# Optimization experiments

Hardware: AMD Instinct MI355X
Metric: run time of the kernel (lower is better)

## Reference

```python
import jax, jax.numpy as jnp
import numpy as np

WH, WW = 8, 8
NUM_HEADS = 8
DIM = 256
MLP_HIDDEN = 1024
EPS = 1e-5


def _rel_pos_index(wh, ww):
    ch, cw = np.meshgrid(np.arange(wh), np.arange(ww), indexing='ij')
    flat = np.stack([ch.ravel(), cw.ravel()])            # (2, N)
    rel = flat[:, :, None] - flat[:, None, :]            # (2, N, N)
    rel = rel.transpose(1, 2, 0).copy()                  # (N, N, 2)
    rel[:, :, 0] += wh - 1
    rel[:, :, 1] += ww - 1
    rel[:, :, 0] *= 2 * ww - 1
    return jnp.asarray(rel.sum(-1))                      # (N, N) int

REL_IDX = _rel_pos_index(WH, WW)


def _layernorm(x, g, b):
    mu = x.mean(-1, keepdims=True)
    var = ((x - mu) ** 2).mean(-1, keepdims=True)
    return (x - mu) * jax.lax.rsqrt(var + EPS) * g + b


def _window_partition(x):
    B, H, W, C = x.shape
    x = x.reshape(B, H // WH, WH, W // WW, WW, C)
    return x.transpose(0, 1, 3, 2, 4, 5).reshape(-1, WH * WW, C)


def _window_reverse(w, B, H, W):
    C = w.shape[-1]
    x = w.reshape(B, H // WH, W // WW, WH, WW, C)
    return x.transpose(0, 1, 3, 2, 4, 5).reshape(B, H, W, C)


def _window_attn(qx, kvx, qw, qb, kvw, kvb, bias_table, pw, pb):
    # qx/kvx: [Bw, N, C]; weights stored as [in, out] (torch Linear transposed)
    Bw, N, C = qx.shape
    hd = C // NUM_HEADS
    scale = hd ** -0.5
    q = (qx @ qw + qb).reshape(Bw, N, NUM_HEADS, hd).transpose(0, 2, 1, 3) * scale
    kv = (kvx @ kvw + kvb).reshape(Bw, N, 2, NUM_HEADS, hd)
    k = kv[:, :, 0].transpose(0, 2, 1, 3)
    v = kv[:, :, 1].transpose(0, 2, 1, 3)
    attn = jnp.einsum('bhnd,bhmd->bhnm', q, k)
    bias = bias_table[REL_IDX.reshape(-1)].reshape(N, N, NUM_HEADS).transpose(2, 0, 1)
    attn = jax.nn.softmax(attn + bias[None], axis=-1)
    out = jnp.einsum('bhnm,bhmd->bhnd', attn, v).transpose(0, 2, 1, 3).reshape(Bw, N, C)
    return out @ pw + pb


def setup_inputs() -> dict:
    key = jax.random.key(0)
    ks = jax.random.split(key, 16)
    B, H, W, C = 4, 160, 160, DIM
    nW = (H // WH) * (W // WW)
    N = WH * WW
    n_bias = (2 * WH - 1) * (2 * WW - 1)  # 225
    s = 0.02
    return {
        'x': jax.random.normal(ks[0], (B, H, W, C), jnp.float32),
        'enc_feat': jax.random.normal(ks[1], (B, H, W, C), jnp.float32),
        'mask_matrix': jnp.zeros((nW, N, N), jnp.float32),
        'norm1_g': jnp.ones((C,), jnp.float32),
        'norm1_b': jnp.zeros((C,), jnp.float32),
        'q1_w': jax.random.normal(ks[2], (C, C), jnp.float32) * s,
        'q1_b': jnp.zeros((C,), jnp.float32),
        'kv1_w': jax.random.normal(ks[3], (C, 2 * C), jnp.float32) * s,
        'kv1_b': jnp.zeros((2 * C,), jnp.float32),
        'bias1': jax.random.normal(ks[4], (n_bias, NUM_HEADS), jnp.float32) * s,
        'proj1_w': jax.random.normal(ks[5], (C, C), jnp.float32) * s,
        'proj1_b': jnp.zeros((C,), jnp.float32),
        'q2_w': jax.random.normal(ks[6], (C, C), jnp.float32) * s,
        'q2_b': jnp.zeros((C,), jnp.float32),
        'kv2_w': jax.random.normal(ks[7], (C, 2 * C), jnp.float32) * s,
        'kv2_b': jnp.zeros((2 * C,), jnp.float32),
        'bias2': jax.random.normal(ks[8], (n_bias, NUM_HEADS), jnp.float32) * s,
        'proj2_w': jax.random.normal(ks[9], (C, C), jnp.float32) * s,
        'proj2_b': jnp.zeros((C,), jnp.float32),
        'norm2_g': jnp.ones((C,), jnp.float32),
        'norm2_b': jnp.zeros((C,), jnp.float32),
        'fc1_w': jax.random.normal(ks[10], (C, MLP_HIDDEN), jnp.float32) * s,
        'fc1_b': jnp.zeros((MLP_HIDDEN,), jnp.float32),
        'fc2_w': jax.random.normal(ks[11], (MLP_HIDDEN, C), jnp.float32) * s,
        'fc2_b': jnp.zeros((C,), jnp.float32),
    }


def reference(x, enc_feat, mask_matrix, norm1_g, norm1_b, q1_w, q1_b, kv1_w, kv1_b,
              bias1, proj1_w, proj1_b, q2_w, q2_b, kv2_w, kv2_b, bias2, proj2_w,
              proj2_b, norm2_g, norm2_b, fc1_w, fc1_b, fc2_w, fc2_b):
    # NOTE: the source forward never passes mask_matrix into attention; faithful here.
    B, H, W, C = x.shape
    shortcut = x
    xn = _layernorm(x, norm1_g, norm1_b)
    xw = _window_partition(xn)              # [B*nW, N, C]
    ew = _window_partition(enc_feat)        # [B*nW, N, C]
    # windowed self-attention with relative position bias
    xw = _window_attn(xw, xw, q1_w, q1_b, kv1_w, kv1_b, bias1, proj1_w, proj1_b)
    # windowed cross-attention to encoder features
    xw = _window_attn(xw, ew, q2_w, q2_b, kv2_w, kv2_b, bias2, proj2_w, proj2_b)
    x = shortcut + _window_reverse(xw, B, H, W)
    h = _layernorm(x, norm2_g, norm2_b)
    h = jax.nn.gelu(h @ fc1_w + fc1_b, approximate=False) @ fc2_w + fc2_b
    return x + h
```

## Files before the change

kernel.cpp:

```cpp
#include <hip/hip_runtime.h>

typedef __attribute__((ext_vector_type(4))) float f32x4;
typedef __attribute__((ext_vector_type(8))) short bf16x8;
typedef __attribute__((ext_vector_type(8))) unsigned short ushort8;
typedef unsigned short u16;
typedef unsigned int u32;

#define LDS_AS(p) ((__attribute__((address_space(3))) void*)(p))
#define GLB_AS(p) ((const __attribute__((address_space(1))) void*)(p))

__device__ __forceinline__ u16 f2b(float f) {
    u32 u = __builtin_bit_cast(u32, f);
    u32 r = (u + 0x7fffu + ((u >> 16) & 1u)) >> 16;
    return (u16)r;
}
__device__ __forceinline__ float b2f(u16 u) {
    return __builtin_bit_cast(float, (u32)u << 16);
}

struct PrepAll {
    const float* src[8];
    u16* dst[8];
    int K[8];
    int N[8];
    float S[8];
};

__global__ __launch_bounds__(256) void prep_w(PrepAll p) {
    const int wi = blockIdx.y;
    const int K = p.K[wi], N = p.N[wi];
    for (int e = blockIdx.x * 256 + threadIdx.x; e < K * N; e += gridDim.x * 256) {
        const int k = e / N, n = e % N;
        p.dst[wi][n * K + k] = f2b(p.src[wi][e] * p.S[wi]);
    }
}

__global__ __launch_bounds__(256) void prep_bias(const float* __restrict__ t1,
                                                 const float* __restrict__ t2,
                                                 float* __restrict__ Bm) {
    const int hh = blockIdx.x;
    const int s = hh >> 3, h = hh & 7;
    const float* tab = s ? t2 : t1;
    const int j = threadIdx.x & 63;
    for (int i = threadIdx.x >> 6; i < 64; i += 4) {
        const int idx = ((i >> 3) - (j >> 3) + 7) * 15 + ((i & 7) - (j & 7) + 7);
        Bm[(long)hh * 4096 + i * 64 + j] = tab[idx * 8 + h];
    }
}

__global__ __launch_bounds__(256) void prep_bcat(const float* __restrict__ q1b,
                                                 const float* __restrict__ q2b,
                                                 float qs, float* __restrict__ q1bs,
                                                 float* __restrict__ q2bs) {
    const int g = threadIdx.x;
    q1bs[g] = qs * q1b[g];
    q2bs[g] = qs * q2b[g];
}

__global__ __launch_bounds__(256) void cast_bf(const float* __restrict__ in,
                                               u16* __restrict__ out, long n8) {
    for (long i = (long)blockIdx.x * 256 + threadIdx.x; i < n8; i += (long)gridDim.x * 256) {
        const float4 a = *(const float4*)(in + i * 8);
        const float4 b = *(const float4*)(in + i * 8 + 4);
        ushort8 o;
        o[0] = f2b(a.x); o[1] = f2b(a.y); o[2] = f2b(a.z); o[3] = f2b(a.w);
        o[4] = f2b(b.x); o[5] = f2b(b.y); o[6] = f2b(b.z); o[7] = f2b(b.w);
        *(ushort8*)(out + i * 8) = o;
    }
}

__global__ __launch_bounds__(256) void ln256(const float* __restrict__ x,
                                             const float* __restrict__ g,
                                             const float* __restrict__ b,
                                             u16* __restrict__ out) {
    const int lane = threadIdx.x & 63;
    const int c = lane * 4;
    const float4 gv = *(const float4*)(g + c);
    const float4 bv = *(const float4*)(b + c);
#pragma unroll
    for (int it = 0; it < 8; ++it) {
        const long row = (long)blockIdx.x * 32 + it * 4 + (threadIdx.x >> 6);
        const float4 v = *(const float4*)(x + row * 256 + c);
        float s = v.x + v.y + v.z + v.w;
        float s2 = v.x * v.x + v.y * v.y + v.z * v.z + v.w * v.w;
#pragma unroll
        for (int off = 32; off > 0; off >>= 1) {
            s += __shfl_xor(s, off);
            s2 += __shfl_xor(s2, off);
        }
        const float mu = s * (1.f / 256.f);
        const float rr = rsqrtf(s2 * (1.f / 256.f) - mu * mu + 1e-5f);
        ushort4 o;
        o.x = f2b((v.x - mu) * rr * gv.x + bv.x);
        o.y = f2b((v.y - mu) * rr * gv.y + bv.y);
        o.z = f2b((v.z - mu) * rr * gv.z + bv.z);
        o.w = f2b((v.w - mu) * rr * gv.w + bv.w);
        *(ushort4*)(out + row * 256 + c) = o;
    }
}

__global__ __launch_bounds__(256) void ln_add(const float* __restrict__ x,
                                              const u16* __restrict__ p,
                                              const float* __restrict__ g,
                                              const float* __restrict__ b,
                                              float* __restrict__ out,
                                              u16* __restrict__ xo) {
    const int lane = threadIdx.x & 63;
    const int c = lane * 4;
    const float4 gv = *(const float4*)(g + c);
    const float4 bv = *(const float4*)(b + c);
#pragma unroll
    for (int it = 0; it < 8; ++it) {
        const long row = (long)blockIdx.x * 32 + it * 4 + (threadIdx.x >> 6);
        float4 v = *(const float4*)(x + row * 256 + c);
        const ushort4 pb = *(const ushort4*)(p + row * 256 + c);
        v.x += b2f(pb.x); v.y += b2f(pb.y); v.z += b2f(pb.z); v.w += b2f(pb.w);
        *(float4*)(out + row * 256 + c) = v;
        float s = v.x + v.y + v.z + v.w;
        float s2 = v.x * v.x + v.y * v.y + v.z * v.z + v.w * v.w;
#pragma unroll
        for (int off = 32; off > 0; off >>= 1) {
            s += __shfl_xor(s, off);
            s2 += __shfl_xor(s2, off);
        }
        const float mu = s * (1.f / 256.f);
        const float rr = rsqrtf(s2 * (1.f / 256.f) - mu * mu + 1e-5f);
        ushort4 o;
        o.x = f2b((v.x - mu) * rr * gv.x + bv.x);
        o.y = f2b((v.y - mu) * rr * gv.y + bv.y);
        o.z = f2b((v.z - mu) * rr * gv.z + bv.z);
        o.w = f2b((v.w - mu) * rr * gv.w + bv.w);
        *(ushort4*)(xo + row * 256 + c) = o;
    }
}

template <int SAME>
__global__ __launch_bounds__(512, 2) void attn_f(const u16* __restrict__ xq,
                                                 const u16* __restrict__ xkv,
                                                 const u16* __restrict__ wq,
                                                 const u16* __restrict__ wkv,
                                                 const float* __restrict__ bq,
                                                 const float* __restrict__ bkv,
                                                 const u16* __restrict__ wp,
                                                 const float* __restrict__ bp,
                                                 const float* __restrict__ Bm,
                                                 u16* __restrict__ OUT) {
    __shared__ u16 LDS[38912];
    const int t = threadIdx.x, lane = t & 63, h = t >> 6;
    const int l15 = lane & 15, lg = lane >> 4;

    const int w = blockIdx.x;
    const int b = w / 400, rem = w % 400;
    const int wy = rem / 20, wx = rem % 20;
    const long base_t = (long)b * 25600 + wy * 1280 + wx * 8;
    auto trow = [&](int r) -> long { return base_t + (r >> 3) * 160 + (r & 7); };

#pragma unroll
    for (int j = 0; j < 4; j++) {
        const int row = j * 16 + (t >> 5);
        const int c0 = t & 31, sc = c0 ^ (row & 7);
        __builtin_amdgcn_global_load_lds(GLB_AS(xq + trow(row) * 256 + sc * 8),
                                         LDS_AS(&LDS[(j * 512 + t) * 8]), 16, 0, 0);
    }
    if (!SAME) {
#pragma unroll
        for (int j = 0; j < 4; j++) {
            const int row = j * 16 + (t >> 5);
            const int c0 = t & 31, sc = c0 ^ (row & 7);
            __builtin_amdgcn_global_load_lds(GLB_AS(xkv + trow(row) * 256 + sc * 8),
                                             LDS_AS(&LDS[16384 + (j * 512 + t) * 8]), 16, 0, 0);
        }
    }
    asm volatile("s_waitcnt vmcnt(0)" ::: "memory");
    __builtin_amdgcn_s_barrier();

    constexpr int XKV = SAME ? 0 : 16384;
    const f32x4 zz = (f32x4){0.f, 0.f, 0.f, 0.f};

    f32x4 aQ[4][2], aK[4][2], aV[4][2];
#pragma unroll
    for (int mi = 0; mi < 4; mi++)
#pragma unroll
        for (int n = 0; n < 2; n++) { aQ[mi][n] = zz; aK[mi][n] = zz; aV[mi][n] = zz; }

    const u16* wv = wkv + 256 * 256;

#define QKV_PASS(ACC, W, XB)                                                               \
    do {                                                                                   \
        _Pragma("unroll") for (int s = 0; s < 8; s++) {                                    \
            bf16x8 wf0 = *(const bf16x8*)((W) + (h * 32 + l15) * 256 + s * 32 + lg * 8);   \
            bf16x8 wf1 = *(const bf16x8*)((W) + (h * 32 + 16 + l15) * 256 + s * 32 + lg * 8); \
            bf16x8 af[4];                                                                  \
            _Pragma("unroll") for (int mi = 0; mi < 4; mi++)                               \
                af[mi] = *(const bf16x8*)&LDS[(XB) + ((mi * 16 + l15) * 32 +               \
                                              ((s * 4 + lg) ^ (l15 & 7))) * 8];            \
            _Pragma("unroll") for (int mi = 0; mi < 4; mi++) {                             \
                ACC[mi][0] = __builtin_amdgcn_mfma_f32_16x16x32_bf16(af[mi], wf0, ACC[mi][0], 0, 0, 0); \
                ACC[mi][1] = __builtin_amdgcn_mfma_f32_16x16x32_bf16(af[mi], wf1, ACC[mi][1], 0, 0, 0); \
            }                                                                              \
        }                                                                                  \
    } while (0)

    QKV_PASS(aQ, wq, 0);
    QKV_PASS(aK, wkv, XKV);
    QKV_PASS(aV, wv, XKV);
#undef QKV_PASS
    __builtin_amdgcn_s_barrier();

    float bQ[2], bK[2], bV[2];
#pragma unroll
    for (int n = 0; n < 2; n++) {
        bQ[n] = bq[h * 32 + n * 16 + l15];
        bK[n] = bkv[h * 32 + n * 16 + l15];
        bV[n] = bkv[256 + h * 32 + n * 16 + l15];
    }

    const int SB = h * 4864;
#pragma unroll
    for (int mi = 0; mi < 4; mi++)
#pragma unroll
        for (int n = 0; n < 2; n++)
#pragma unroll
            for (int r = 0; r < 4; r++)
                LDS[SB + 2560 + (n * 16 + l15) * 72 + mi * 16 + lg * 4 + r] = f2b(aV[mi][n][r] + bV[n]);

#pragma unroll
    for (int mi = 0; mi < 4; mi++)
#pragma unroll
        for (int n = 0; n < 2; n++)
#pragma unroll
            for (int r = 0; r < 4; r++)
                LDS[SB + (mi * 16 + lg * 4 + r) * 40 + n * 16 + l15] = f2b(aQ[mi][n][r] + bQ[n]);
    bf16x8 qf[4];
#pragma unroll
    for (int ti = 0; ti < 4; ti++)
        qf[ti] = *(const bf16x8*)&LDS[SB + (ti * 16 + l15) * 40 + lg * 8];
#pragma unroll
    for (int mi = 0; mi < 4; mi++)
#pragma unroll
        for (int n = 0; n < 2; n++)
#pragma unroll
            for (int r = 0; r < 4; r++)
                LDS[SB + (mi * 16 + lg * 4 + r) * 40 + n * 16 + l15] = f2b(aK[mi][n][r] + bK[n]);
    bf16x8 kf[4];
#pragma unroll
    for (int ti = 0; ti < 4; ti++)
        kf[ti] = *(const bf16x8*)&LDS[SB + (ti * 16 + l15) * 40 + lg * 8];

    f32x4 s4[4][4];
#pragma unroll
    for (int ti = 0; ti < 4; ti++)
#pragma unroll
        for (int tj = 0; tj < 4; tj++)
            s4[ti][tj] = __builtin_amdgcn_mfma_f32_16x16x32_bf16(qf[ti], kf[tj], zz, 0, 0, 0);

    const float* Bh = Bm + h * 4096;
    f32x4 o[4][2];
#pragma unroll
    for (int mi = 0; mi < 4; mi++)
#pragma unroll
        for (int n = 0; n < 2; n++) o[mi][n] = zz;

#pragma unroll
    for (int hf = 0; hf < 2; ++hf) {
#pragma unroll
        for (int ti = 0; ti < 4; ti++) {
#pragma unroll
            for (int r = 0; r < 4; r++) {
                const int i = ti * 16 + lg * 4 + r;
                float vv[4];
                float m = -1e30f;
#pragma unroll
                for (int tj = 0; tj < 4; tj++) {
                    vv[tj] = s4[ti][tj][r] + Bh[i * 64 + tj * 16 + l15];
                    m = fmaxf(m, vv[tj]);
                }
#pragma unroll
                for (int off = 1; off < 16; off <<= 1) m = fmaxf(m, __shfl_xor(m, off));
                float sum = 0.f;
#pragma unroll
                for (int tj = 0; tj < 4; tj++) {
                    vv[tj] = __expf(vv[tj] - m);
                    sum += vv[tj];
                }
#pragma unroll
                for (int off = 1; off < 16; off <<= 1) sum += __shfl_xor(sum, off);
                const float inv = 1.f / sum;
#pragma unroll
                for (int u = 0; u < 2; u++)
                    LDS[SB + i * 40 + u * 16 + l15] = f2b(vv[hf * 2 + u] * inv);
            }
        }
        bf16x8 vf[2];
#pragma unroll
        for (int n = 0; n < 2; n++)
            vf[n] = *(const bf16x8*)&LDS[SB + 2560 + (n * 16 + l15) * 72 + hf * 32 + lg * 8];
#pragma unroll
        for (int mi = 0; mi < 4; mi++) {
            bf16x8 pf = *(const bf16x8*)&LDS[SB + (mi * 16 + l15) * 40 + lg * 8];
#pragma unroll
            for (int n = 0; n < 2; n++)
                o[mi][n] = __builtin_amdgcn_mfma_f32_16x16x32_bf16(pf, vf[n], o[mi][n], 0, 0, 0);
        }
    }

    __builtin_amdgcn_s_barrier();
#pragma unroll
    for (int mi = 0; mi < 4; mi++)
#pragma unroll
        for (int n = 0; n < 2; n++)
#pragma unroll
            for (int r = 0; r < 4; r++)
                LDS[(mi * 16 + lg * 4 + r) * 264 + h * 32 + n * 16 + l15] = f2b(o[mi][n][r]);
    __builtin_amdgcn_s_barrier();

    bf16x8 pwf[2][8];
#pragma unroll
    for (int n = 0; n < 2; n++)
#pragma unroll
        for (int s = 0; s < 8; s++)
            pwf[n][s] = *(const bf16x8*)(wp + (h * 32 + n * 16 + l15) * 256 + s * 32 + lg * 8);
    f32x4 pacc[4][2];
#pragma unroll
    for (int mi = 0; mi < 4; mi++)
#pragma unroll
        for (int n = 0; n < 2; n++) pacc[mi][n] = zz;
#pragma unroll
    for (int s = 0; s < 8; s++) {
        bf16x8 paf[4];
#pragma unroll
        for (int mi = 0; mi < 4; mi++)
            paf[mi] = *(const bf16x8*)&LDS[(mi * 16 + l15) * 264 + s * 32 + lg * 8];
#pragma unroll
        for (int mi = 0; mi < 4; mi++)
#pragma unroll
            for (int n = 0; n < 2; n++)
                pacc[mi][n] = __builtin_amdgcn_mfma_f32_16x16x32_bf16(paf[mi], pwf[n][s], pacc[mi][n], 0, 0, 0);
    }
    float pb2[2];
#pragma unroll
    for (int n = 0; n < 2; n++) pb2[n] = bp[h * 32 + n * 16 + l15];
#pragma unroll
    for (int mi = 0; mi < 4; mi++)
#pragma unroll
        for (int n = 0; n < 2; n++)
#pragma unroll
            for (int r = 0; r < 4; r++) {
                const int i = mi * 16 + lg * 4 + r;
                OUT[trow(i) * 256 + h * 32 + n * 16 + l15] = f2b(pacc[mi][n][r] + pb2[n]);
            }
}

__global__ __launch_bounds__(512, 2) void mlpf(const u16* __restrict__ xo,
                                               const u16* __restrict__ w1,
                                               const float* __restrict__ b1,
                                               const u16* __restrict__ w2,
                                               const float* __restrict__ b2,
                                               float* __restrict__ out) {
    __shared__ u16 W[32768];
    __shared__ u16 HS[8192];
    const int t = threadIdx.x, lane = t & 63, h = t >> 6;
    const int l15 = lane & 15, lg = lane >> 4;
    const long r0 = (long)blockIdx.x * 128 + h * 16;
    const f32x4 zz = (f32x4){0.f, 0.f, 0.f, 0.f};

    bf16x8 af[8];
#pragma unroll
    for (int s = 0; s < 8; s++)
        af[s] = *(const bf16x8*)(xo + (r0 + l15) * 256 + s * 32 + lg * 8);

    f32x4 yacc[16];
#pragma unroll
    for (int n = 0; n < 16; n++) yacc[n] = zz;

    const int hsb = h * 1024;

    for (int c = 0; c < 16; ++c) {
        if (c) __builtin_amdgcn_s_barrier();
#pragma unroll
        for (int rnd = 0; rnd < 4; rnd++) {
            const int ia = rnd * 512 + t;
            const int rowa = ia >> 5, sca = (ia & 31) ^ (rowa & 7);
            __builtin_amdgcn_global_load_lds(GLB_AS(w1 + (c * 64 + rowa) * 256 + sca * 8),
                                             LDS_AS(&W[ia * 8]), 16, 0, 0);
        }
#pragma unroll
        for (int rnd = 0; rnd < 4; rnd++) {
            const int ib = rnd * 512 + t;
            const int rowb = ib >> 3, scb = (ib & 7) ^ (rowb & 7);
            __builtin_amdgcn_global_load_lds(GLB_AS(w2 + rowb * 1024 + c * 64 + scb * 8),
                                             LDS_AS(&W[16384 + ib * 8]), 16, 0, 0);
        }
        asm volatile("s_waitcnt vmcnt(0)" ::: "memory");
        __builtin_amdgcn_s_barrier();

        float f1bb[4];
#pragma unroll
        for (int n = 0; n < 4; n++) f1bb[n] = b1[c * 64 + n * 16 + l15];

        f32x4 hc[4];
#pragma unroll
        for (int n = 0; n < 4; n++) hc[n] = zz;
#pragma unroll
        for (int s = 0; s < 8; s++) {
            bf16x8 bf[4];
#pragma unroll
            for (int n = 0; n < 4; n++)
                bf[n] = *(const bf16x8*)&W[((n * 16 + l15) * 32 + ((s * 4 + lg) ^ (l15 & 7))) * 8];
#pragma unroll
            for (int n = 0; n < 4; n++)
                hc[n] = __builtin_amdgcn_mfma_f32_16x16x32_bf16(af[s], bf[n], hc[n], 0, 0, 0);
        }
#pragma unroll
        for (int n = 0; n < 4; n++)
#pragma unroll
            for (int r = 0; r < 4; r++) {
                float v = hc[n][r] + f1bb[n];
                v = 0.5f * v * (1.f + erff(v * 0.70710678118f));
                const int row = lg * 4 + r;
                HS[hsb + row * 64 + ((n * 16 + l15) ^ ((row & 7) << 3))] = f2b(v);
            }

#pragma unroll
        for (int ks = 0; ks < 2; ks++) {
            bf16x8 haf = *(const bf16x8*)&HS[hsb + l15 * 64 + ((ks * 32 + lg * 8) ^ ((l15 & 7) << 3))];
            bf16x8 bf2[16];
#pragma unroll
            for (int n = 0; n < 16; n++)
                bf2[n] = *(const bf16x8*)&W[16384 + ((n * 16 + l15) * 8 + ((ks * 4 + lg) ^ (l15 & 7))) * 8];
#pragma unroll
            for (int n = 0; n < 16; n++)
                yacc[n] = __builtin_amdgcn_mfma_f32_16x16x32_bf16(haf, bf2[n], yacc[n], 0, 0, 0);
        }
    }

    float f2bb[16];
#pragma unroll
    for (int n = 0; n < 16; n++) f2bb[n] = b2[n * 16 + l15];
#pragma unroll
    for (int n = 0; n < 16; n++)
#pragma unroll
        for (int r = 0; r < 4; r++) {
            const long idx = (r0 + lg * 4 + r) * 256 + n * 16 + l15;
            out[idx] = yacc[n][r] + f2bb[n] + out[idx];
        }
}

extern "C" void kernel_launch(void* const* d_in, const int* in_sizes, int n_in,
                              void* d_out, int out_size, void* d_ws, size_t ws_size,
                              hipStream_t stream) {
    const float* x    = (const float*)d_in[0];
    const float* enc  = (const float*)d_in[1];
    const float* n1g  = (const float*)d_in[3];
    const float* n1b  = (const float*)d_in[4];
    const float* q1w  = (const float*)d_in[5];
    const float* q1b  = (const float*)d_in[6];
    const float* kv1w = (const float*)d_in[7];
    const float* kv1b = (const float*)d_in[8];
    const float* bias1 = (const float*)d_in[9];
    const float* p1w  = (const float*)d_in[10];
    const float* p1b  = (const float*)d_in[11];
    const float* q2w  = (const float*)d_in[12];
    const float* q2b  = (const float*)d_in[13];
    const float* kv2w = (const float*)d_in[14];
    const float* kv2b = (const float*)d_in[15];
    const float* bias2 = (const float*)d_in[16];
    const float* p2w  = (const float*)d_in[17];
    const float* p2bi = (const float*)d_in[18];
    const float* n2g  = (const float*)d_in[19];
    const float* n2b  = (const float*)d_in[20];
    const float* f1w  = (const float*)d_in[21];
    const float* f1b  = (const float*)d_in[22];
    const float* f2w  = (const float*)d_in[23];
    const float* f2bias = (const float*)d_in[24];
    float* out = (float*)d_out;

    char* ws = (char*)d_ws;
    size_t off = 0;
    auto alloc = [&](size_t bytes) {
        char* p = ws + off;
        off += (bytes + 255) & ~(size_t)255;
        return p;
    };
    u16* Wt    = (u16*)alloc(1048576 * 2);
    float* Bm  = (float*)alloc(16 * 4096 * 4);
    float* q1s = (float*)alloc(256 * 4);
    float* q2s = (float*)alloc(256 * 4);
    u16* xn    = (u16*)alloc(52428800);
    u16* y1    = (u16*)alloc(52428800);
    u16* pj2   = (u16*)alloc(52428800);
    u16* encb  = (u16*)alloc(52428800);

    u16 *q1t = Wt, *kv1t = Wt + 65536, *p1t = Wt + 196608, *q2t = Wt + 262144,
        *kv2t = Wt + 327680, *p2t = Wt + 458752, *f1t = Wt + 524288, *f2t = Wt + 786432;

    const float qscale = 0.17677669529663687f;

    PrepAll pa;
    pa.src[0] = q1w;  pa.dst[0] = q1t;  pa.K[0] = 256;  pa.N[0] = 256;  pa.S[0] = qscale;
    pa.src[1] = kv1w; pa.dst[1] = kv1t; pa.K[1] = 256;  pa.N[1] = 512;  pa.S[1] = 1.f;
    pa.src[2] = p1w;  pa.dst[2] = p1t;  pa.K[2] = 256;  pa.N[2] = 256;  pa.S[2] = 1.f;
    pa.src[3] = q2w;  pa.dst[3] = q2t;  pa.K[3] = 256;  pa.N[3] = 256;  pa.S[3] = qscale;
    pa.src[4] = kv2w; pa.dst[4] = kv2t; pa.K[4] = 256;  pa.N[4] = 512;  pa.S[4] = 1.f;
    pa.src[5] = p2w;  pa.dst[5] = p2t;  pa.K[5] = 256;  pa.N[5] = 256;  pa.S[5] = 1.f;
    pa.src[6] = f1w;  pa.dst[6] = f1t;  pa.K[6] = 256;  pa.N[6] = 1024; pa.S[6] = 1.f;
    pa.src[7] = f2w;  pa.dst[7] = f2t;  pa.K[7] = 1024; pa.N[7] = 256;  pa.S[7] = 1.f;
    prep_w<<<dim3(128, 8), 256, 0, stream>>>(pa);
    prep_bias<<<dim3(16), 256, 0, stream>>>(bias1, bias2, Bm);
    prep_bcat<<<dim3(1), 256, 0, stream>>>(q1b, q2b, qscale, q1s, q2s);
    cast_bf<<<dim3(2048), 256, 0, stream>>>(enc, encb, 3276800);
    ln256<<<dim3(3200), 256, 0, stream>>>(x, n1g, n1b, xn);

    attn_f<1><<<dim3(1600), 512, 0, stream>>>(xn, xn, q1t, kv1t, q1s, kv1b,
                                              p1t, p1b, Bm, y1);
    attn_f<0><<<dim3(1600), 512, 0, stream>>>(y1, encb, q2t, kv2t, q2s, kv2b,
                                              p2t, p2bi, Bm + 8 * 4096, pj2);

    ln_add<<<dim3(3200), 256, 0, stream>>>(x, pj2, n2g, n2b, out, xn);

    mlpf<<<dim3(800), 512, 0, stream>>>(xn, f1t, f1b, f2t, f2bias, out);
}
```

Before: 902.2 us.

## Double-buffer MLP weight chunks and hoist QKV weight fragments into registers

The fused MLP kernel now streams fc1/fc2 weight chunks of 32 hidden units into two LDS buffers. The next-but-one chunk is prefetched while the current one is computed, with a partial vmcnt wait, so global loads overlap with MFMA work. The hidden-activation scratch switches from an XOR swizzle to a padded stride. Separately, the QKV projection loads all weight fragments for a pass into registers before issuing MFMAs. This trades higher register pressure and more barriers per chunk for latency hiding.

```diff
diff --git a/kernel.cpp b/kernel.cpp
--- a/kernel.cpp
+++ b/kernel.cpp
@@ -16,6 +16,13 @@
 }
 __device__ __forceinline__ float b2f(u16 u) {
     return __builtin_bit_cast(float, (u32)u << 16);
+}
+
+__device__ __forceinline__ void vmwait(int n) {
+    if (n == 0)
+        asm volatile("s_waitcnt vmcnt(0)" ::: "memory");
+    else
+        asm volatile("s_waitcnt vmcnt(4)" ::: "memory");
 }
 
 struct PrepAll {
@@ -185,20 +192,21 @@
 
     const u16* wv = wkv + 256 * 256;
 
-#define QKV_PASS(ACC, W, XB)                                                               \
-    do {                                                                                   \
-        _Pragma("unroll") for (int s = 0; s < 8; s++) {                                    \
-            bf16x8 wf0 = *(const bf16x8*)((W) + (h * 32 + l15) * 256 + s * 32 + lg * 8);   \
-            bf16x8 wf1 = *(const bf16x8*)((W) + (h * 32 + 16 + l15) * 256 + s * 32 + lg * 8); \
-            bf16x8 af[4];                                                                  \
-            _Pragma("unroll") for (int mi = 0; mi < 4; mi++)                               \
-                af[mi] = *(const bf16x8*)&LDS[(XB) + ((mi * 16 + l15) * 32 +               \
-                                              ((s * 4 + lg) ^ (l15 & 7))) * 8];            \
-            _Pragma("unroll") for (int mi = 0; mi < 4; mi++) {                             \
-                ACC[mi][0] = __builtin_amdgcn_mfma_f32_16x16x32_bf16(af[mi], wf0, ACC[mi][0], 0, 0, 0); \
-                ACC[mi][1] = __builtin_amdgcn_mfma_f32_16x16x32_bf16(af[mi], wf1, ACC[mi][1], 0, 0, 0); \
-            }                                                                              \
-        }                                                                                  \
+#define QKV_PASS(ACC, W, XB)                                                              \
+    do {                                                                                  \
+        bf16x8 wf[2][8];                                                                  \
+        _Pragma("unroll") for (int n = 0; n < 2; n++)                                     \
+            _Pragma("unroll") for (int s = 0; s < 8; s++)                                 \
+                wf[n][s] = *(const bf16x8*)((W) + (h * 32 + n * 16 + l15) * 256 + s * 32 + lg * 8); \
+        _Pragma("unroll") for (int s = 0; s < 8; s++) {                                   \
+            bf16x8 af[4];                                                                 \
+            _Pragma("unroll") for (int mi = 0; mi < 4; mi++)                              \
+                af[mi] = *(const bf16x8*)&LDS[(XB) + ((mi * 16 + l15) * 32 +              \
+                                              ((s * 4 + lg) ^ (l15 & 7))) * 8];           \
+            _Pragma("unroll") for (int mi = 0; mi < 4; mi++)                              \
+                _Pragma("unroll") for (int n = 0; n < 2; n++)                             \
+                    ACC[mi][n] = __builtin_amdgcn_mfma_f32_16x16x32_bf16(af[mi], wf[n][s], ACC[mi][n], 0, 0, 0); \
+        }                                                                                 \
     } while (0)
 
     QKV_PASS(aQ, wq, 0);
@@ -357,8 +365,8 @@
                                                const u16* __restrict__ w2,
                                                const float* __restrict__ b2,
                                                float* __restrict__ out) {
-    __shared__ u16 W[32768];
-    __shared__ u16 HS[8192];
+    __shared__ u16 W[2][16384];
+    __shared__ u16 HS[8][640];
     const int t = threadIdx.x, lane = t & 63, h = t >> 6;
     const int l15 = lane & 15, lg = lane >> 4;
     const long r0 = (long)blockIdx.x * 128 + h * 16;
@@ -373,65 +381,69 @@
 #pragma unroll
     for (int n = 0; n < 16; n++) yacc[n] = zz;
 
-    const int hsb = h * 1024;
-
-    for (int c = 0; c < 16; ++c) {
-        if (c) __builtin_amdgcn_s_barrier();
-#pragma unroll
-        for (int rnd = 0; rnd < 4; rnd++) {
+    auto stage = [&](int c, int buf) {
+#pragma unroll
+        for (int rnd = 0; rnd < 2; rnd++) {
             const int ia = rnd * 512 + t;
             const int rowa = ia >> 5, sca = (ia & 31) ^ (rowa & 7);
-            __builtin_amdgcn_global_load_lds(GLB_AS(w1 + (c * 64 + rowa) * 256 + sca * 8),
-                                             LDS_AS(&W[ia * 8]), 16, 0, 0);
-        }
-#pragma unroll
-        for (int rnd = 0; rnd < 4; rnd++) {
+            __builtin_amdgcn_global_load_lds(GLB_AS(w1 + (c * 32 + rowa) * 256 + sca * 8),
+                                             LDS_AS(&W[buf][ia * 8]), 16, 0, 0);
+        }
+#pragma unroll
+        for (int rnd = 0; rnd < 2; rnd++) {
             const int ib = rnd * 512 + t;
-            const int rowb = ib >> 3, scb = (ib & 7) ^ (rowb & 7);
-            __builtin_amdgcn_global_load_lds(GLB_AS(w2 + rowb * 1024 + c * 64 + scb * 8),
-                                             LDS_AS(&W[16384 + ib * 8]), 16, 0, 0);
-        }
-        asm volatile("s_waitcnt vmcnt(0)" ::: "memory");
+            const int rowb = ib >> 2, kc = (ib & 3) ^ ((rowb >> 1) & 3);
+            __builtin_amdgcn_global_load_lds(GLB_AS(w2 + rowb * 1024 + c * 32 + kc * 8),
+                                             LDS_AS(&W[buf][8192 + ib * 8]), 16, 0, 0);
+        }
+    };
+
+    stage(0, 0);
+    stage(1, 1);
+
+    for (int c = 0; c < 32; ++c) {
+        const int buf = c & 1;
+        vmwait(c < 31 ? 4 : 0);
         __builtin_amdgcn_s_barrier();
 
-        float f1bb[4];
-#pragma unroll
-        for (int n = 0; n < 4; n++) f1bb[n] = b1[c * 64 + n * 16 + l15];
-
-        f32x4 hc[4];
-#pragma unroll
-        for (int n = 0; n < 4; n++) hc[n] = zz;
+        float f1bb[2];
+#pragma unroll
+        for (int n = 0; n < 2; n++) f1bb[n] = b1[c * 32 + n * 16 + l15];
+
+        f32x4 hc[2];
+#pragma unroll
+        for (int n = 0; n < 2; n++) hc[n] = zz;
 #pragma unroll
         for (int s = 0; s < 8; s++) {
-            bf16x8 bf[4];
-#pragma unroll
-            for (int n = 0; n < 4; n++)
-                bf[n] = *(const bf16x8*)&W[((n * 16 + l15) * 32 + ((s * 4 + lg) ^ (l15 & 7))) * 8];
-#pragma unroll
-            for (int n = 0; n < 4; n++)
+            bf16x8 bf[2];
+#pragma unroll
+            for (int n = 0; n < 2; n++)
+                bf[n] = *(const bf16x8*)&W[buf][((n * 16 + l15) * 32 + ((s * 4 + lg) ^ (l15 & 7))) * 8];
+#pragma unroll
+            for (int n = 0; n < 2; n++)
                 hc[n] = __builtin_amdgcn_mfma_f32_16x16x32_bf16(af[s], bf[n], hc[n], 0, 0, 0);
         }
 #pragma unroll
-        for (int n = 0; n < 4; n++)
+        for (int n = 0; n < 2; n++)
 #pragma unroll
             for (int r = 0; r < 4; r++) {
                 float v = hc[n][r] + f1bb[n];
                 v = 0.5f * v * (1.f + erff(v * 0.70710678118f));
-                const int row = lg * 4 + r;
-                HS[hsb + row * 64 + ((n * 16 + l15) ^ ((row & 7) << 3))] = f2b(v);
+                HS[h][(lg * 4 + r) * 40 + n * 16 + l15] = f2b(v);
             }
 
-#pragma unroll
-        for (int ks = 0; ks < 2; ks++) {
-            bf16x8 haf = *(const bf16x8*)&HS[hsb + l15 * 64 + ((ks * 32 + lg * 8) ^ ((l15 & 7) << 3))];
-            bf16x8 bf2[16];
-#pragma unroll
-            for (int n = 0; n < 16; n++)
-                bf2[n] = *(const bf16x8*)&W[16384 + ((n * 16 + l15) * 8 + ((ks * 4 + lg) ^ (l15 & 7))) * 8];
-#pragma unroll
-            for (int n = 0; n < 16; n++)
-                yacc[n] = __builtin_amdgcn_mfma_f32_16x16x32_bf16(haf, bf2[n], yacc[n], 0, 0, 0);
-        }
+        {
+            bf16x8 haf = *(const bf16x8*)&HS[h][l15 * 40 + lg * 8];
+#pragma unroll
+            for (int n = 0; n < 16; n++) {
+                const int row = n * 16 + l15;
+                bf16x8 bf2 = *(const bf16x8*)&W[buf][8192 + (row * 4 + (lg ^ ((row >> 1) & 3))) * 8];
+                yacc[n] = __builtin_amdgcn_mfma_f32_16x16x32_bf16(haf, bf2, yacc[n], 0, 0, 0);
+            }
+        }
+
+        __builtin_amdgcn_s_barrier();
+        if (c + 2 < 32) stage(c + 2, buf);
     }
 
     float f2bb[16];
```

New measurement: 862.6 us. -4.4%, faster.
